# Kernel tuning notes

Measured on AMD Instinct MI355X. Metric: run time of the kernel, lower is better.

The kernel has to match this reference:

```python
import jax, jax.numpy as jnp
import numpy as np

C, D, B = 32768, 1024, 16384
LABEL = 0.95  # EMA keep factor from __init__ default


def setup_inputs() -> dict:
    key = jax.random.key(0)
    k1, k2, k3, k4 = jax.random.split(key, 4)
    return {
        "s_logits": jax.random.normal(k1, (C, D), dtype=jnp.float32),
        "t_logits": jax.random.normal(k2, (C, D), dtype=jnp.float32),
        "logits": jax.random.normal(k3, (B, D), dtype=jnp.float32),
        "the_class": jax.random.randint(k4, (B,), 0, C, dtype=jnp.int64),
    }


def _ema_scatter(table, logits, the_class, keep):
    """Sequential per-row EMA: for i in range(B): table[c_i] = table[c_i]*keep + logits[i]*(1-keep).
    Vectorized: row c with k occurrences -> table[c]*keep^k + (1-keep)*sum_j keep^{#later occurrences} * logits[j].
    """
    Bn = the_class.shape[0]
    Cn = table.shape[0]
    dt = table.dtype
    ones = jnp.ones((Bn,), dtype=dt)
    counts = jax.ops.segment_sum(ones, the_class, num_segments=Cn)  # [C]
    # occurrence rank (0-based, in original batch order) of each sample within its class
    order = jnp.argsort(the_class)  # stable sort preserves batch order within a class
    sc = the_class[order]
    first = jnp.searchsorted(sc, sc, side="left")  # start of each class segment
    rank_sorted = jnp.arange(Bn, dtype=jnp.int32) - first.astype(jnp.int32)
    rank = jnp.zeros((Bn,), jnp.int32).at[order].set(rank_sorted)
    # number of later same-class occurrences
    r = counts[the_class] - 1.0 - rank.astype(dt)  # [B]
    w = (1.0 - keep) * jnp.power(jnp.asarray(keep, dt), r)  # [B]
    contrib = jax.ops.segment_sum(logits * w[:, None], the_class, num_segments=Cn)  # [C, D]
    decay = jnp.power(jnp.asarray(keep, dt), counts)  # [C]; rows absent from batch keep decay=1
    return table * decay[:, None] + contrib


def reference(s_logits, t_logits, logits, the_class):
    new_s = _ema_scatter(s_logits, logits, the_class, LABEL)  # update(type='s')
    loss = jnp.mean(jnp.sum(jnp.abs(new_s - t_logits), axis=1))  # loss()
    return loss
```

## Files before the change

### kernel.cpp

```cpp
#include <hip/hip_runtime.h>

#define NC 32768
#define ND 1024
#define NQ 256
#define NB 16384
#define KEEP 0.95f
#define OMK  0.05f
#define KCAP 16
#define JPAD 2
#define RPB  4

typedef float fx4 __attribute__((ext_vector_type(4)));

__global__ void count_scatter_kernel(const int* __restrict__ the_class,
                                     int* __restrict__ counts,
                                     int* __restrict__ idx_list) {
    int i = blockIdx.x * blockDim.x + threadIdx.x;
    if (i < NB) {
        int c = the_class[i];
        int pos = atomicAdd(&counts[c], 1);
        if (pos < KCAP) idx_list[c * KCAP + pos] = i;
    }
}

__global__ void wprep_kernel(const int* __restrict__ counts,
                             const int* __restrict__ idx_list,
                             float* __restrict__ decays,
                             int2* __restrict__ elist) {
    int c = blockIdx.x * blockDim.x + threadIdx.x;
    int cnt = counts[c];
    float base = KEEP, r = 1.0f;
    for (int e = cnt; e > 0; e >>= 1) { if (e & 1) r *= base; base *= base; }
    decays[c] = r;
    int m = cnt < KCAP ? cnt : KCAP;
    int idx[KCAP];
    for (int j = 0; j < m; ++j) idx[j] = idx_list[c * KCAP + j];
    for (int j = 0; j < KCAP; ++j) {
        int2 e;
        if (j < m) {
            int later = 0;
            for (int l = 0; l < m; ++l) later += (idx[l] > idx[j]);
            float w = OMK;
            for (int k = 0; k < later; ++k) w *= KEEP;
            e.x = idx[j]; e.y = __float_as_int(w);
        } else {
            e.x = 0; e.y = __float_as_int(0.0f);
        }
        elist[c * KCAP + j] = e;
    }
}

__global__ __launch_bounds__(256) void loss_kernel(
    const float* __restrict__ s_logits,
    const float* __restrict__ t_logits,
    const float* __restrict__ logits,
    const int*   __restrict__ counts,
    const float* __restrict__ decays,
    const int2*  __restrict__ elist,
    float* __restrict__ out) {

    const int q  = threadIdx.x;
    const int c0 = blockIdx.x * RPB;

    const fx4* s4 = (const fx4*)s_logits;
    const fx4* t4 = (const fx4*)t_logits;
    const fx4* l4 = (const fx4*)logits;

    float dec[RPB]; int m[RPB]; int2 ge[RPB][JPAD];
    #pragma unroll
    for (int r = 0; r < RPB; ++r) {
        dec[r] = decays[c0 + r];
        int cnt = counts[c0 + r];
        m[r] = cnt < KCAP ? cnt : KCAP;
        #pragma unroll
        for (int j = 0; j < JPAD; ++j) ge[r][j] = elist[(c0 + r) * KCAP + j];
    }

    fx4 sv[RPB], tv[RPB], gv[RPB][JPAD];
    #pragma unroll
    for (int r = 0; r < RPB; ++r)
        sv[r] = __builtin_nontemporal_load(&s4[(size_t)(c0 + r) * NQ + q]);
    #pragma unroll
    for (int r = 0; r < RPB; ++r)
        tv[r] = __builtin_nontemporal_load(&t4[(size_t)(c0 + r) * NQ + q]);
    #pragma unroll
    for (int r = 0; r < RPB; ++r) {
        #pragma unroll
        for (int j = 0; j < JPAD; ++j)
            gv[r][j] = l4[(size_t)ge[r][j].x * NQ + q];
    }

    float lsum = 0.0f;
    #pragma unroll
    for (int r = 0; r < RPB; ++r) {
        fx4 acc = sv[r] * dec[r];
        #pragma unroll
        for (int j = 0; j < JPAD; ++j) {
            const float w = __int_as_float(ge[r][j].y);
            acc.x = fmaf(w, gv[r][j].x, acc.x);
            acc.y = fmaf(w, gv[r][j].y, acc.y);
            acc.z = fmaf(w, gv[r][j].z, acc.z);
            acc.w = fmaf(w, gv[r][j].w, acc.w);
        }
        if (m[r] > JPAD) {
            for (int j = JPAD; j < m[r]; ++j) {
                int2 e = elist[(c0 + r) * KCAP + j];
                const float w = __int_as_float(e.y);
                fx4 lv = l4[(size_t)e.x * NQ + q];
                acc.x = fmaf(w, lv.x, acc.x);
                acc.y = fmaf(w, lv.y, acc.y);
                acc.z = fmaf(w, lv.z, acc.z);
                acc.w = fmaf(w, lv.w, acc.w);
            }
        }
        lsum += fabsf(acc.x - tv[r].x) + fabsf(acc.y - tv[r].y) +
                fabsf(acc.z - tv[r].z) + fabsf(acc.w - tv[r].w);
    }

    #pragma unroll
    for (int off = 32; off > 0; off >>= 1) lsum += __shfl_down(lsum, off);
    __shared__ float wsum[4];
    const int wave = threadIdx.x >> 6, lane = threadIdx.x & 63;
    if (lane == 0) wsum[wave] = lsum;
    __syncthreads();
    if (threadIdx.x == 0) {
        float total = (wsum[0] + wsum[1] + wsum[2] + wsum[3]) * (1.0f / NC);
        atomicAdd(out, total);
    }
}

extern "C" void kernel_launch(void* const* d_in, const int* in_sizes, int n_in,
                              void* d_out, int out_size, void* d_ws, size_t ws_size,
                              hipStream_t stream) {
    const float* s_logits  = (const float*)d_in[0];
    const float* t_logits  = (const float*)d_in[1];
    const float* logits    = (const float*)d_in[2];
    const int*   the_class = (const int*)d_in[3];
    float* out = (float*)d_out;

    int*   counts   = (int*)d_ws;
    int*   idx_list = counts + NC;
    float* decays   = (float*)(idx_list + NC * KCAP);
    int2*  elist    = (int2*)(decays + NC);

    (void)hipMemsetAsync(counts, 0, NC * sizeof(int), stream);
    (void)hipMemsetAsync(d_out, 0, sizeof(float), stream);

    count_scatter_kernel<<<NB / 256, 256, 0, stream>>>(the_class, counts, idx_list);
    wprep_kernel<<<NC / 256, 256, 0, stream>>>(counts, idx_list, decays, elist);
    loss_kernel<<<NC / RPB, 256, 0, stream>>>(s_logits, t_logits, logits,
                                              counts, decays, elist, out);
}
```

Measured before the change: 358.2 us.

## Pack per-group gather entries and software-pipeline loss kernel over groups

Entries are now grouped per 4-row group into a compacted list tagged with the row index, so each group prefetches a fixed number of gathered logits rows shared across its 4 rows instead of 2 slots per row. The loss kernel becomes persistent over 8 groups per block with double-buffered metadata and data loads, so the next group's loads are issued while the current group computes. The changes aim to cut wasted padded gathers and hide memory latency. The cost is extra masked FMAs and higher register pressure, and nontemporal loads were dropped.

```diff
diff --git a/kernel.cpp b/kernel.cpp
--- a/kernel.cpp
+++ b/kernel.cpp
@@ -7,8 +7,12 @@
 #define KEEP 0.95f
 #define OMK  0.05f
 #define KCAP 16
-#define JPAD 2
-#define RPB  4
+#define RPG  4
+#define NG   (NC / RPG)
+#define GCAP 6
+#define GMAX 64
+#define ITERS 8
+#define NBLK (NG / ITERS)
 
 typedef float fx4 __attribute__((ext_vector_type(4)));
 
@@ -23,98 +27,133 @@
     }
 }
 
-__global__ void wprep_kernel(const int* __restrict__ counts,
-                             const int* __restrict__ idx_list,
-                             float* __restrict__ decays,
-                             int2* __restrict__ elist) {
-    int c = blockIdx.x * blockDim.x + threadIdx.x;
-    int cnt = counts[c];
-    float base = KEEP, r = 1.0f;
-    for (int e = cnt; e > 0; e >>= 1) { if (e & 1) r *= base; base *= base; }
-    decays[c] = r;
-    int m = cnt < KCAP ? cnt : KCAP;
-    int idx[KCAP];
-    for (int j = 0; j < m; ++j) idx[j] = idx_list[c * KCAP + j];
-    for (int j = 0; j < KCAP; ++j) {
-        int2 e;
-        if (j < m) {
+__global__ void wprep_group_kernel(const int* __restrict__ counts,
+                                   const int* __restrict__ idx_list,
+                                   float* __restrict__ decays,
+                                   int* __restrict__ group_n,
+                                   int2* __restrict__ group_all) {
+    int g = blockIdx.x * blockDim.x + threadIdx.x;
+    if (g >= NG) return;
+    int n = 0;
+    for (int r = 0; r < RPG; ++r) {
+        int c = g * RPG + r;
+        int cnt = counts[c];
+        float base = KEEP, dr = 1.0f;
+        for (int e = cnt; e > 0; e >>= 1) { if (e & 1) dr *= base; base *= base; }
+        decays[c] = dr;
+        int m = cnt < KCAP ? cnt : KCAP;
+        int idx[KCAP];
+        for (int j = 0; j < m; ++j) idx[j] = idx_list[c * KCAP + j];
+        for (int j = 0; j < m; ++j) {
             int later = 0;
             for (int l = 0; l < m; ++l) later += (idx[l] > idx[j]);
             float w = OMK;
             for (int k = 0; k < later; ++k) w *= KEEP;
-            e.x = idx[j]; e.y = __float_as_int(w);
-        } else {
-            e.x = 0; e.y = __float_as_int(0.0f);
+            int2 e; e.x = idx[j] | (r << 16); e.y = __float_as_int(w);
+            if (n < GMAX) group_all[(size_t)g * GMAX + n] = e;
+            n++;
         }
-        elist[c * KCAP + j] = e;
     }
+    int real = n < GMAX ? n : GMAX;
+    for (int j = real; j < GCAP; ++j) {
+        int2 e; e.x = 0; e.y = 0;
+        group_all[(size_t)g * GMAX + j] = e;
+    }
+    group_n[g] = real;
 }
 
-__global__ __launch_bounds__(256) void loss_kernel(
+__global__ __launch_bounds__(256, 2) void loss_kernel(
     const float* __restrict__ s_logits,
     const float* __restrict__ t_logits,
     const float* __restrict__ logits,
-    const int*   __restrict__ counts,
     const float* __restrict__ decays,
-    const int2*  __restrict__ elist,
+    const int*   __restrict__ group_n,
+    const int2*  __restrict__ group_all,
     float* __restrict__ out) {
 
     const int q  = threadIdx.x;
-    const int c0 = blockIdx.x * RPB;
+    const int g0 = blockIdx.x * ITERS;
 
     const fx4* s4 = (const fx4*)s_logits;
     const fx4* t4 = (const fx4*)t_logits;
     const fx4* l4 = (const fx4*)logits;
+    const float4* dec4p = (const float4*)decays;
 
-    float dec[RPB]; int m[RPB]; int2 ge[RPB][JPAD];
-    #pragma unroll
-    for (int r = 0; r < RPB; ++r) {
-        dec[r] = decays[c0 + r];
-        int cnt = counts[c0 + r];
-        m[r] = cnt < KCAP ? cnt : KCAP;
+    float4 dec[2]; int gn[2]; int2 ent[2][GCAP];
+    fx4 sv[2][RPG], tv[2][RPG], gv[2][GCAP];
+
+    auto loadMeta = [&](int gi, int p) {
+        dec[p] = dec4p[gi];
+        gn[p]  = group_n[gi];
         #pragma unroll
-        for (int j = 0; j < JPAD; ++j) ge[r][j] = elist[(c0 + r) * KCAP + j];
-    }
-
-    fx4 sv[RPB], tv[RPB], gv[RPB][JPAD];
-    #pragma unroll
-    for (int r = 0; r < RPB; ++r)
-        sv[r] = __builtin_nontemporal_load(&s4[(size_t)(c0 + r) * NQ + q]);
-    #pragma unroll
-    for (int r = 0; r < RPB; ++r)
-        tv[r] = __builtin_nontemporal_load(&t4[(size_t)(c0 + r) * NQ + q]);
-    #pragma unroll
-    for (int r = 0; r < RPB; ++r) {
+        for (int j = 0; j < GCAP; ++j)
+            ent[p][j] = group_all[(size_t)gi * GMAX + j];
+    };
+    auto issueData = [&](int gi, int p) {
         #pragma unroll
-        for (int j = 0; j < JPAD; ++j)
-            gv[r][j] = l4[(size_t)ge[r][j].x * NQ + q];
-    }
+        for (int r = 0; r < RPG; ++r)
+            sv[p][r] = s4[(gi * RPG + r) * NQ + q];
+        #pragma unroll
+        for (int r = 0; r < RPG; ++r)
+            tv[p][r] = t4[(gi * RPG + r) * NQ + q];
+        #pragma unroll
+        for (int j = 0; j < GCAP; ++j)
+            gv[p][j] = l4[(ent[p][j].x & 0xffff) * NQ + q];
+    };
 
     float lsum = 0.0f;
+    loadMeta(g0, 0);
+    loadMeta(g0 + 1, 1);
+    issueData(g0, 0);
+
     #pragma unroll
-    for (int r = 0; r < RPB; ++r) {
-        fx4 acc = sv[r] * dec[r];
+    for (int i = 0; i < ITERS; ++i) {
+        const int p = i & 1;
+        if (i + 1 < ITERS) issueData(g0 + i + 1, (i + 1) & 1);
+
+        fx4 acc[RPG];
+        const float dd[RPG] = {dec[p].x, dec[p].y, dec[p].z, dec[p].w};
         #pragma unroll
-        for (int j = 0; j < JPAD; ++j) {
-            const float w = __int_as_float(ge[r][j].y);
-            acc.x = fmaf(w, gv[r][j].x, acc.x);
-            acc.y = fmaf(w, gv[r][j].y, acc.y);
-            acc.z = fmaf(w, gv[r][j].z, acc.z);
-            acc.w = fmaf(w, gv[r][j].w, acc.w);
-        }
-        if (m[r] > JPAD) {
-            for (int j = JPAD; j < m[r]; ++j) {
-                int2 e = elist[(c0 + r) * KCAP + j];
-                const float w = __int_as_float(e.y);
-                fx4 lv = l4[(size_t)e.x * NQ + q];
-                acc.x = fmaf(w, lv.x, acc.x);
-                acc.y = fmaf(w, lv.y, acc.y);
-                acc.z = fmaf(w, lv.z, acc.z);
-                acc.w = fmaf(w, lv.w, acc.w);
+        for (int r = 0; r < RPG; ++r) acc[r] = sv[p][r] * dd[r];
+
+        #pragma unroll
+        for (int j = 0; j < GCAP; ++j) {
+            const int   rw = ent[p][j].x >> 16;
+            const float w  = __int_as_float(ent[p][j].y);
+            #pragma unroll
+            for (int r = 0; r < RPG; ++r) {
+                const float we = (rw == r) ? w : 0.0f;
+                acc[r].x = fmaf(we, gv[p][j].x, acc[r].x);
+                acc[r].y = fmaf(we, gv[p][j].y, acc[r].y);
+                acc[r].z = fmaf(we, gv[p][j].z, acc[r].z);
+                acc[r].w = fmaf(we, gv[p][j].w, acc[r].w);
             }
         }
-        lsum += fabsf(acc.x - tv[r].x) + fabsf(acc.y - tv[r].y) +
-                fabsf(acc.z - tv[r].z) + fabsf(acc.w - tv[r].w);
+        const int n = gn[p];
+        if (n > GCAP) {
+            for (int j = GCAP; j < n; ++j) {
+                int2 e = group_all[(size_t)(g0 + i) * GMAX + j];
+                const int   rw = e.x >> 16;
+                const float w  = __int_as_float(e.y);
+                fx4 lv = l4[(e.x & 0xffff) * NQ + q];
+                #pragma unroll
+                for (int r = 0; r < RPG; ++r) {
+                    const float we = (rw == r) ? w : 0.0f;
+                    acc[r].x = fmaf(we, lv.x, acc[r].x);
+                    acc[r].y = fmaf(we, lv.y, acc[r].y);
+                    acc[r].z = fmaf(we, lv.z, acc[r].z);
+                    acc[r].w = fmaf(we, lv.w, acc[r].w);
+                }
+            }
+        }
+
+        if (i + 2 < ITERS) loadMeta(g0 + i + 2, p);
+
+        #pragma unroll
+        for (int r = 0; r < RPG; ++r) {
+            lsum += fabsf(acc[r].x - tv[p][r].x) + fabsf(acc[r].y - tv[p][r].y) +
+                    fabsf(acc[r].z - tv[p][r].z) + fabsf(acc[r].w - tv[p][r].w);
+        }
     }
 
     #pragma unroll
@@ -138,16 +177,18 @@
     const int*   the_class = (const int*)d_in[3];
     float* out = (float*)d_out;
 
-    int*   counts   = (int*)d_ws;
-    int*   idx_list = counts + NC;
-    float* decays   = (float*)(idx_list + NC * KCAP);
-    int2*  elist    = (int2*)(decays + NC);
+    int*   counts    = (int*)d_ws;
+    int*   idx_list  = counts + NC;
+    float* decays    = (float*)(idx_list + NC * KCAP);
+    int*   group_n   = (int*)(decays + NC);
+    int2*  group_all = (int2*)(group_n + NG);
 
     (void)hipMemsetAsync(counts, 0, NC * sizeof(int), stream);
     (void)hipMemsetAsync(d_out, 0, sizeof(float), stream);
 
     count_scatter_kernel<<<NB / 256, 256, 0, stream>>>(the_class, counts, idx_list);
-    wprep_kernel<<<NC / 256, 256, 0, stream>>>(counts, idx_list, decays, elist);
-    loss_kernel<<<NC / RPB, 256, 0, stream>>>(s_logits, t_logits, logits,
-                                              counts, decays, elist, out);
+    wprep_group_kernel<<<NG / 256, 256, 0, stream>>>(counts, idx_list, decays,
+                                                     group_n, group_all);
+    loss_kernel<<<NBLK, 256, 0, stream>>>(s_logits, t_logits, logits,
+                                          decays, group_n, group_all, out);
 }
```

Result: no change. 363.1 us (+1.4%).
